# Performance work log

Measured on AMD Instinct MI355X. Metric: run time of the kernel, lower is better.

## Reference

```python
import jax, jax.numpy as jnp
import numpy as np

N_PTS = 200000
N_EDGES = 1600000
REL_W = 7          # 1 tex col + 2 slots of (vx, vy, tex_rt)
MEM_W = 63         # quantization: values in [0, 63]
LIN_RAD = 1.0
N_ROLL = 5
MEM_SIZE = 2 ** 27 # dense emulation of the sparse COO count memory
MASK = (MEM_SIZE // 64) - 1  # for modular base-64 Horner hashing


def setup_inputs() -> dict:
    key = jax.random.key(0)
    k1, k2, k3 = jax.random.split(key, 3)
    pts = jax.random.uniform(k1, (N_PTS, 2), dtype=jnp.float32)
    tex = jax.random.uniform(k2, (N_PTS, 1), dtype=jnp.float32)
    edges = jax.random.randint(k3, (N_EDGES, 2), 0, N_PTS, dtype=jnp.int64)
    mem = jnp.zeros((MEM_SIZE,), dtype=jnp.float32)
    return {"pts": pts, "tex": tex, "edges": edges, "mem": mem}


def _build_rel(pts, tex, edges):
    # filter_thresh: binarize texture at 0.7
    tex_b = (tex[:, 0] > 0.7).astype(jnp.int32)            # [N]
    # symmetrize edge list (frnn returns one direction)
    e = jnp.concatenate([edges, edges[:, ::-1]], axis=0)   # [E, 2]
    src, dst = e[:, 0], e[:, 1]
    # quantized relative displacement vectors
    d = pts[dst] - pts[src]                                # [E, 2]
    vecs = jnp.clip(jnp.round(((d / LIN_RAD) + 1.0) / 2.0 * MEM_W), 0, MEM_W).astype(jnp.int32)
    tex_rt = tex_b[dst]                                    # [E]
    # occurrence rank of each edge within its source row (== write_cols logic)
    E = src.shape[0]
    order = jnp.argsort(src, stable=True)
    sr = src[order]
    idx = jnp.arange(E, dtype=jnp.int32)
    is_start = jnp.concatenate([jnp.array([True]), sr[1:] != sr[:-1]])
    seg_start = jax.lax.associative_scan(jnp.maximum, jnp.where(is_start, idx, 0))
    occ = jnp.zeros(E, jnp.int32).at[order].set(idx - seg_start)
    # only the first (REL_W-1)//3 slots per row fit; others are skipped
    valid = occ < (REL_W - 1) // 3
    col = 1 + 3 * occ
    N = pts.shape[0]
    wrow = jnp.where(valid, src, N)  # out-of-range row -> dropped by scatter
    rel = jnp.zeros((N, REL_W), jnp.int32).at[:, 0].set(tex_b)
    rel = rel.at[wrow, col].set(vecs[:, 0], mode='drop')
    rel = rel.at[wrow, col + 1].set(vecs[:, 1], mode='drop')
    rel = rel.at[wrow, col + 2].set(tex_rt, mode='drop')
    return rel


def _roll_rel(rel, n_roll):
    # home tex (col 0) stays; remaining cols roll by 3*i
    rolled = [jnp.concatenate([rel[:, :1], jnp.roll(rel[:, 1:], 3 * i, axis=1)], axis=1)
              for i in range(n_roll + 1)]
    return jnp.concatenate(rolled, axis=0)


def _hash_rows(rel_all):
    # base-64 Horner hash mod 2^27 (emulates sparse COO multi-index)
    v = jnp.clip(rel_all, 0, MEM_W)  # each column in [0, 63]
    acc = jnp.zeros(rel_all.shape[0], jnp.int32)
    for j in range(REL_W - 1, -1, -1):
        acc = (acc & MASK) * 64 + v[:, j]
    return acc


def reference(pts, tex, edges, mem):
    rel0 = _roll_rel(_build_rel(pts, tex, edges), N_ROLL)
    rel1 = _roll_rel(_build_rel(pts, tex, edges), N_ROLL)
    rel_all = jnp.concatenate([rel0, rel1], axis=0)        # [2*(n_roll+1)*N, REL_W]
    flat = _hash_rows(rel_all)
    # mem.add_(sparse_coo(ones at rel_vec indices)) -> scatter-add count histogram
    return mem.at[flat].add(1.0)
```

## Files before the change

### kernel.cpp

```cpp
#include <hip/hip_runtime.h>

#define N_PTS   200000
#define N_EDGES 1600000
#define MEM_SIZE (1 << 27)

#define NP   16
#define NPB  12800
#define EP   16
#define EPS  (N_EDGES / EP)
#define EPS4 (EPS / 2)
#define NBLK (NP * EP)
#define NTHR 1024
#define NF4  (MEM_SIZE / 4)
#define CSTRIDE (NBLK * NTHR)
#define CITER (NF4 / CSTRIDE)
#define SITER ((EPS4 + NTHR - 1) / NTHR)

__device__ __forceinline__ void upd2(unsigned* __restrict__ mn1, unsigned* __restrict__ mn2,
                                     int a, unsigned i) {
    if ((unsigned)a < NPB) {
        unsigned old = atomicMin(&mn1[a], i);
        unsigned c = (i < old) ? old : i;
        atomicMin(&mn2[a], c);
    }
}

__device__ __forceinline__ void proc(unsigned* __restrict__ mn1, unsigned* __restrict__ mn2,
                                     int lo, int4 p, int g ) {
    unsigned ia0 = (unsigned)(2 * g);
    unsigned ib0 = (unsigned)(2 * g + N_EDGES);
    upd2(mn1, mn2, p.x - lo, ia0);
    upd2(mn1, mn2, p.y - lo, ib0);
    upd2(mn1, mn2, p.z - lo, ia0 + 1u);
    upd2(mn1, mn2, p.w - lo, ib0 + 1u);
}

__global__ __launch_bounds__(NTHR) void fused_copy_scan(const float4* __restrict__ src,
                                                        float4* __restrict__ dst,
                                                        const int4* __restrict__ edges4,
                                                        unsigned long long* __restrict__ W) {
    __shared__ unsigned mn1[NPB];
    __shared__ unsigned mn2[NPB];

    int b  = blockIdx.x;
    int ep = b & 15;
    int np = b >> 4;
    int lo = np * NPB;
    int t  = threadIdx.x;

    for (int j = t; j < NPB; j += NTHR) { mn1[j] = 0xFFFFFFFFu; mn2[j] = 0xFFFFFFFFu; }
    __syncthreads();

    int q0 = ep * EPS4;
    int cbase = b * NTHR + t;

    #pragma unroll 8
    for (int j = 0; j < CITER; ++j) {
        int ci = cbase + j * CSTRIDE;
        float4 v = src[ci];
        int k = t + j * NTHR;
        bool have = (j < SITER) && (k < EPS4);
        int4 p;
        if (have) p = edges4[q0 + k];
        dst[ci] = v;
        if (have) proc(mn1, mn2, lo, p, q0 + k);
    }
    __syncthreads();

    for (int j = t; j < NPB; j += NTHR) {
        int n = lo + j;
        if (n < N_PTS)
            W[(size_t)ep * N_PTS + n] =
                ((unsigned long long)mn2[j] << 32) | (unsigned long long)mn1[j];
    }
}

__device__ __forceinline__ int quant6(float d) {
    float x = ((d + 1.0f) / 2.0f) * 63.0f;
    float r = rintf(x);
    r = fminf(fmaxf(r, 0.0f), 63.0f);
    return (int)r;
}

__global__ void finalize(const float* __restrict__ pts, const float* __restrict__ tex,
                         const int2* __restrict__ edges,
                         const unsigned long long* __restrict__ W,
                         float* __restrict__ out) {
    int n = blockIdx.x * blockDim.x + threadIdx.x;
    if (n >= N_PTS) return;

    unsigned int k1 = 0xFFFFFFFFu, k2 = 0xFFFFFFFFu;
    #pragma unroll
    for (int s = 0; s < EP; ++s) {
        unsigned long long pr = W[(size_t)s * N_PTS + n];
        unsigned int m1 = (unsigned int)(pr & 0xFFFFFFFFu);
        unsigned int m2 = (unsigned int)(pr >> 32);
        if (m1 < k1) { k2 = k1; k1 = m1; } else if (m1 < k2) { k2 = m1; }
        if (m2 < k2 && m2 > k1) { k2 = m2; }
    }

    float px = pts[2 * n], py = pts[2 * n + 1];
    int t = (tex[n] > 0.7f) ? 1 : 0;

    int v0x = 0, v0y = 0, t0 = 0, v1x = 0, v1y = 0, t1 = 0;

    if (k1 < 2u * N_EDGES) {
        int k = (int)k1;
        int2 e = edges[(k < N_EDGES) ? k : (k - N_EDGES)];
        int dst = (k < N_EDGES) ? e.y : e.x;
        v0x = quant6(pts[2 * dst] - px);
        v0y = quant6(pts[2 * dst + 1] - py);
        t0 = (tex[dst] > 0.7f) ? 1 : 0;
    }
    if (k2 < 2u * N_EDGES) {
        int k = (int)k2;
        int2 e = edges[(k < N_EDGES) ? k : (k - N_EDGES)];
        int dst = (k < N_EDGES) ? e.y : e.x;
        v1x = quant6(pts[2 * dst] - px);
        v1y = quant6(pts[2 * dst + 1] - py);
        t1 = (tex[dst] > 0.7f) ? 1 : 0;
    }

    int h_id = t | (v0x << 6) | (v0y << 12) | (t0 << 18) | ((v1x & 7) << 24);
    int h_sw = t | (v1x << 6) | (v1y << 12) | (t1 << 18) | ((v0x & 7) << 24);

    atomicAdd(&out[h_id], 6.0f);
    atomicAdd(&out[h_sw], 6.0f);
}

extern "C" void kernel_launch(void* const* d_in, const int* in_sizes, int n_in,
                              void* d_out, int out_size, void* d_ws, size_t ws_size,
                              hipStream_t stream) {
    const float* pts   = (const float*)d_in[0];
    const float* tex   = (const float*)d_in[1];
    const int2*  edges = (const int2*)d_in[2];
    const float* mem   = (const float*)d_in[3];
    float*       out   = (float*)d_out;

    unsigned long long* W = (unsigned long long*)d_ws;

    fused_copy_scan<<<NBLK, NTHR, 0, stream>>>(
        (const float4*)mem, (float4*)out, (const int4*)edges, W);
    finalize<<<(N_PTS + 255) / 256, 256, 0, stream>>>(pts, tex, edges, W, out);
}
```

Before: 237.4 us.

## Warp-specialize fused kernel: scan waves and copy waves, then finish copy after barrier

Each block now splits its threads. The first 256 threads do the edge scan and shared-memory atomic min updates, unrolled 4-way. The remaining 768 threads copy a contiguous per-block chunk of the memory buffer. After the barrier, all threads finish the rest of the block's copy share with a contiguous layout. The aim is to overlap the latency-bound atomic scan with the bandwidth-bound copy rather than interleaving them in the same threads, at the risk of a load imbalance between the two roles.

```diff
diff --git a/kernel.cpp b/kernel.cpp
--- a/kernel.cpp
+++ b/kernel.cpp
@@ -12,9 +12,12 @@
 #define NBLK (NP * EP)
 #define NTHR 1024
 #define NF4  (MEM_SIZE / 4)
-#define CSTRIDE (NBLK * NTHR)
-#define CITER (NF4 / CSTRIDE)
-#define SITER ((EPS4 + NTHR - 1) / NTHR)
+#define SHARE (NF4 / NBLK)
+#define SCAN_L 256
+#define CPY_A  768
+#define ITER_A 44
+#define OFF_B  (CPY_A * ITER_A)
+#define ITER_B ((SHARE - OFF_B) / NTHR)
 
 __device__ __forceinline__ void upd2(unsigned* __restrict__ mn1, unsigned* __restrict__ mn2,
                                      int a, unsigned i) {
@@ -51,19 +54,29 @@
     for (int j = t; j < NPB; j += NTHR) { mn1[j] = 0xFFFFFFFFu; mn2[j] = 0xFFFFFFFFu; }
     __syncthreads();
 
-    int q0 = ep * EPS4;
-    int cbase = b * NTHR + t;
-
-    #pragma unroll 8
-    for (int j = 0; j < CITER; ++j) {
-        int ci = cbase + j * CSTRIDE;
-        float4 v = src[ci];
-        int k = t + j * NTHR;
-        bool have = (j < SITER) && (k < EPS4);
-        int4 p;
-        if (have) p = edges4[q0 + k];
-        dst[ci] = v;
-        if (have) proc(mn1, mn2, lo, p, q0 + k);
+    if (t < SCAN_L) {
+        int q0 = ep * EPS4;
+        int k = t;
+        for (; k + 3 * SCAN_L < EPS4; k += 4 * SCAN_L) {
+            int4 p0 = edges4[q0 + k];
+            int4 p1 = edges4[q0 + k + SCAN_L];
+            int4 p2 = edges4[q0 + k + 2 * SCAN_L];
+            int4 p3 = edges4[q0 + k + 3 * SCAN_L];
+            proc(mn1, mn2, lo, p0, q0 + k);
+            proc(mn1, mn2, lo, p1, q0 + k + SCAN_L);
+            proc(mn1, mn2, lo, p2, q0 + k + 2 * SCAN_L);
+            proc(mn1, mn2, lo, p3, q0 + k + 3 * SCAN_L);
+        }
+        for (; k < EPS4; k += SCAN_L) {
+            int4 p = edges4[q0 + k];
+            proc(mn1, mn2, lo, p, q0 + k);
+        }
+    } else {
+        int u  = t - SCAN_L;
+        int cb = b * SHARE + u;
+        #pragma unroll 4
+        for (int i = 0; i < ITER_A; ++i)
+            dst[cb + i * CPY_A] = src[cb + i * CPY_A];
     }
     __syncthreads();
 
@@ -73,6 +86,11 @@
             W[(size_t)ep * N_PTS + n] =
                 ((unsigned long long)mn2[j] << 32) | (unsigned long long)mn1[j];
     }
+
+    int cb = b * SHARE + OFF_B + t;
+    #pragma unroll 4
+    for (int i = 0; i < ITER_B; ++i)
+        dst[cb + i * NTHR] = src[cb + i * NTHR];
 }
 
 __device__ __forceinline__ int quant6(float d) {
```

New measurement: 293.1 us. 23.5% more time.
